# Performance work log

Hardware: AMD Instinct MI355X
Metric: run time of the kernel (lower is better)

The kernel has to match this reference:

```python
import jax, jax.numpy as jnp
import numpy as np

B, T, E, C, H = 8, 96, 96, 256, 8
D = C // H
HID = int(C * 4.0)
EPS = 1e-5


def _ln(x, g, b):
    m = x.mean(-1, keepdims=True)
    v = ((x - m) ** 2).mean(-1, keepdims=True)
    return (x - m) * jax.lax.rsqrt(v + EPS) * g + b


def setup_inputs() -> dict:
    key = jax.random.key(0)
    ks = jax.random.split(key, 20)
    s = 0.02
    inp = {
        "x": jax.random.normal(ks[0], (B, T, E, C), jnp.float32),
        "adj_mask": jax.random.uniform(ks[1], (E, E), jnp.float32) * 2.0 - 1.0,  # direction cosines in [-1,1]
        "n1_g": jnp.ones((C,)), "n1_b": jnp.zeros((C,)),
        "s_wq": jax.random.normal(ks[2], (C, C)) * s,
        "s_wk": jax.random.normal(ks[3], (C, C)) * s,
        "s_wv": jax.random.normal(ks[4], (C, C)) * s,
        "s_wp": jax.random.normal(ks[5], (C, C)) * s,
        "s_bp": jnp.zeros((C,)),
        "s_ng": jnp.ones((C,)), "s_nb": jnp.zeros((C,)),
        "s_gamma": jax.random.normal(ks[6], (1,)) * 0.1,
        "n2_g": jnp.ones((C,)), "n2_b": jnp.zeros((C,)),
        "t_wq": jax.random.normal(ks[7], (C, C)) * s,
        "t_wk": jax.random.normal(ks[8], (C, C)) * s,
        "t_wv": jax.random.normal(ks[9], (C, C)) * s,
        "t_wp": jax.random.normal(ks[10], (C, C)) * s,
        "t_bp": jnp.zeros((C,)),
        "t_gamma": jax.random.normal(ks[11], (1,)) * 0.1,
        "n3_g": jnp.ones((C,)), "n3_b": jnp.zeros((C,)),
        "m_w1": jax.random.normal(ks[12], (C, HID)) * s,
        "m_b1": jnp.zeros((HID,)),
        "m_w2": jax.random.normal(ks[13], (HID, C)) * s,
        "m_b2": jnp.zeros((C,)),
    }
    return inp


def _interp_linear_T(x, t_new):
    # x: [B, T, E, C]; torch F.interpolate(mode='linear', align_corners=False) over T
    t = x.shape[1]
    scale = t / t_new
    src = (jnp.arange(t_new, dtype=jnp.float32) + 0.5) * scale - 0.5
    src = jnp.clip(src, 0.0, t - 1)
    i0 = jnp.floor(src).astype(jnp.int32)
    i1 = jnp.minimum(i0 + 1, t - 1)
    w = (src - i0.astype(jnp.float32))[None, :, None, None]
    return x[:, i0] * (1.0 - w) + x[:, i1] * w


def reference(x, adj_mask, n1_g, n1_b, s_wq, s_wk, s_wv, s_wp, s_bp, s_ng, s_nb, s_gamma,
              n2_g, n2_b, t_wq, t_wk, t_wv, t_wp, t_bp, t_gamma,
              n3_g, n3_b, m_w1, m_b1, m_w2, m_b2):
    b, t, e, c = x.shape
    h, d = H, C // H

    # ---- spatial geometric-cosine attention (per frame) ----
    xs = _ln(x, n1_g, n1_b)                                    # identity inside spatial_attn
    q = (xs @ s_wq).reshape(b, t, e, h, d)
    k = (xs @ s_wk).reshape(b, t, e, h, d)
    v = (xs @ s_wv).reshape(b, t, e, h, d)
    attn = jnp.einsum('btqhd,btkhd->bthqk', q, k)
    attn = (attn * adj_mask + 1.0) * 0.5                        # masked-cosine, no softmax
    o = jnp.einsum('bthqk,btkhd->btqhd', attn, v).reshape(b, t, e, c)
    o = _ln(o @ s_wp + s_bp, s_ng, s_nb)
    x = x + (xs + s_gamma * o)

    # ---- temporal softmax attention (per edge) ----
    xt = _ln(x, n2_g, n2_b)
    q = (xt @ t_wq).reshape(b, t, e, h, d)
    k = (xt @ t_wk).reshape(b, t, e, h, d)
    v = (xt @ t_wv).reshape(b, t, e, h, d)
    attn = jnp.einsum('bqehd,bkehd->behqk', q, k) * (d ** -0.5)
    attn = jax.nn.softmax(attn, axis=-1)
    o = jnp.einsum('behqk,bkehd->bqehd', attn, v).reshape(b, t, e, c)
    o = o @ t_wp + t_bp
    x = x + t_gamma * o

    # ---- MLP ----
    xm = _ln(x, n3_g, n3_b)
    x = x + (jax.nn.gelu(xm @ m_w1 + m_b1, approximate=False) @ m_w2 + m_b2)

    # ---- temporal downsampling (interpolate) ----
    t_new = t // 2 + t % 2
    if t > 1:
        x = _interp_linear_T(x, t_new)
    return x
```

## Files before the change

### kernel.cpp

```cpp
#include <hip/hip_runtime.h>
#include <cmath>

constexpr int BB = 8, TT = 96, EE = 96, CC = 256, HHD = 8, DDm = 32;
constexpr int NTOK = BB * TT * EE;
constexpr int TOUT = TT / 2;

typedef unsigned short u16;
typedef short bf16x8 __attribute__((ext_vector_type(8)));
typedef float f32x4 __attribute__((ext_vector_type(4)));

__device__ __forceinline__ float bf2f(u16 u) {
  union { unsigned int i; float f; } v; v.i = ((unsigned int)u) << 16; return v.f;
}
__device__ __forceinline__ u16 f2bf(float f) {
  union { unsigned int i; float f; } v; v.f = f;
  return (u16)((v.i + 0x7FFFu + ((v.i >> 16) & 1u)) >> 16);
}
__device__ __forceinline__ float wsum(float v) {
#pragma unroll
  for (int off = 32; off; off >>= 1) v += __shfl_xor(v, off);
  return v;
}
__device__ __forceinline__ float gelu_f(float x) {
  return 0.5f * x * (1.0f + erff(x * 0.70710678118654752f));
}
__device__ __forceinline__ int remap_row(int row, int mode) {
  if (mode == 0) return row;
  int b = row / (TT * EE);
  int rem = row - b * (TT * EE);
  if (mode == 1) { int t = rem / EE, e = rem - t * EE; return (b * EE + e) * TT + t; }
  int e = rem / TT, t = rem - e * TT;
  return (b * TT + t) * EE + e;
}

struct WPtr8 { const float* p[8]; };
__global__ void k_transpose8(WPtr8 src, u16* __restrict__ dst) {
  const float* in = src.p[blockIdx.y];
  u16* out = dst + (size_t)blockIdx.y * 65536;
  int idx = blockIdx.x * 256 + threadIdx.x;
  int k = idx >> 8, c = idx & 255;
  out[c * 256 + k] = f2bf(in[idx]);
}

__global__ void k_transpose(const float* __restrict__ in, u16* __restrict__ out, int K, int Nc, int n) {
  int idx = blockIdx.x * 256 + threadIdx.x;
  if (idx < n) {
    int k = idx / Nc, c = idx - k * Nc;
    out[c * K + k] = f2bf(in[idx]);
  }
}

__global__ void k_cvt(const float* __restrict__ in, u16* __restrict__ out, int n) {
  int idx = blockIdx.x * 256 + threadIdx.x;
  if (idx < n) out[idx] = f2bf(in[idx]);
}

__global__ __launch_bounds__(256) void k_ln_in(const float* __restrict__ x,
                                               u16* __restrict__ A, const float* __restrict__ g,
                                               const float* __restrict__ b) {
  int wv = threadIdx.x >> 6, lane = threadIdx.x & 63;
  long tok = (long)blockIdx.x * 4 + wv;
  int c = lane * 4;
  long off = tok * CC + c;
  float4 v = *(const float4*)(x + off);
  float s = v.x + v.y + v.z + v.w;
  float sq = v.x * v.x + v.y * v.y + v.z * v.z + v.w * v.w;
  s = wsum(s); sq = wsum(sq);
  float m = s * (1.0f / CC);
  float rs = rsqrtf(sq * (1.0f / CC) - m * m + 1e-5f);
  float4 gv = *(const float4*)(g + c);
  float4 bv = *(const float4*)(b + c);
  ushort4 o;
  o.x = f2bf((v.x - m) * rs * gv.x + bv.x);
  o.y = f2bf((v.y - m) * rs * gv.y + bv.y);
  o.z = f2bf((v.z - m) * rs * gv.z + bv.z);
  o.w = f2bf((v.w - m) * rs * gv.w + bv.w);
  *(ushort4*)(A + off) = o;
}

__global__ __launch_bounds__(256) void k_ln_f32(const float* __restrict__ X, u16* __restrict__ A,
                                                const float* __restrict__ g, const float* __restrict__ b) {
  int wv = threadIdx.x >> 6, lane = threadIdx.x & 63;
  long tok = (long)blockIdx.x * 4 + wv;
  int c = lane * 4;
  long off = tok * CC + c;
  float4 v = *(const float4*)(X + off);
  float s = v.x + v.y + v.z + v.w;
  float sq = v.x * v.x + v.y * v.y + v.z * v.z + v.w * v.w;
  s = wsum(s); sq = wsum(sq);
  float m = s * (1.0f / CC);
  float rs = rsqrtf(sq * (1.0f / CC) - m * m + 1e-5f);
  float4 gv = *(const float4*)(g + c);
  float4 bv = *(const float4*)(b + c);
  ushort4 o;
  o.x = f2bf((v.x - m) * rs * gv.x + bv.x);
  o.y = f2bf((v.y - m) * rs * gv.y + bv.y);
  o.z = f2bf((v.z - m) * rs * gv.z + bv.z);
  o.w = f2bf((v.w - m) * rs * gv.w + bv.w);
  *(ushort4*)(A + off) = o;
}

__global__ __launch_bounds__(256) void k_sp_combine(const float* __restrict__ xin, float* __restrict__ X,
                                                    u16* __restrict__ A, const u16* __restrict__ P,
                                                    const float* __restrict__ n1g, const float* __restrict__ n1b,
                                                    const float* __restrict__ sg,
                                                    const float* __restrict__ s_ng, const float* __restrict__ s_nb,
                                                    const float* __restrict__ n2g, const float* __restrict__ n2b) {
  int wv = threadIdx.x >> 6, lane = threadIdx.x & 63;
  long tok = (long)blockIdx.x * 4 + wv;
  int c = lane * 4;
  long off = tok * CC + c;
  float4 xv = *(const float4*)(xin + off);
  float s1 = xv.x + xv.y + xv.z + xv.w;
  float q1 = xv.x * xv.x + xv.y * xv.y + xv.z * xv.z + xv.w * xv.w;
  s1 = wsum(s1); q1 = wsum(q1);
  float m1 = s1 * (1.0f / CC);
  float r1 = rsqrtf(q1 * (1.0f / CC) - m1 * m1 + 1e-5f);
  float4 g1 = *(const float4*)(n1g + c);
  float4 b1 = *(const float4*)(n1b + c);
  float xs0 = (xv.x - m1) * r1 * g1.x + b1.x;
  float xs1 = (xv.y - m1) * r1 * g1.y + b1.y;
  float xs2 = (xv.z - m1) * r1 * g1.z + b1.z;
  float xs3 = (xv.w - m1) * r1 * g1.w + b1.w;
  ushort4 up = *(const ushort4*)(P + off);
  float4 p = make_float4(bf2f(up.x), bf2f(up.y), bf2f(up.z), bf2f(up.w));
  float s = p.x + p.y + p.z + p.w;
  float sq = p.x * p.x + p.y * p.y + p.z * p.z + p.w * p.w;
  s = wsum(s); sq = wsum(sq);
  float m = s * (1.0f / CC);
  float rs = rsqrtf(sq * (1.0f / CC) - m * m + 1e-5f);
  float4 ug = *(const float4*)(s_ng + c);
  float4 ub = *(const float4*)(s_nb + c);
  float o0 = (p.x - m) * rs * ug.x + ub.x;
  float o1 = (p.y - m) * rs * ug.y + ub.y;
  float o2 = (p.z - m) * rs * ug.z + ub.z;
  float o3 = (p.w - m) * rs * ug.w + ub.w;
  float gsg = sg[0];
  float x0 = xv.x + xs0 + gsg * o0;
  float x1 = xv.y + xs1 + gsg * o1;
  float x2 = xv.z + xs2 + gsg * o2;
  float x3 = xv.w + xs3 + gsg * o3;
  *(float4*)(X + off) = make_float4(x0, x1, x2, x3);
  float s2 = x0 + x1 + x2 + x3;
  float sq2 = x0 * x0 + x1 * x1 + x2 * x2 + x3 * x3;
  s2 = wsum(s2); sq2 = wsum(sq2);
  float m2 = s2 * (1.0f / CC);
  float rs2 = rsqrtf(sq2 * (1.0f / CC) - m2 * m2 + 1e-5f);
  float4 g2 = *(const float4*)(n2g + c);
  float4 b2 = *(const float4*)(n2b + c);
  ushort4 o;
  o.x = f2bf((x0 - m2) * rs2 * g2.x + b2.x);
  o.y = f2bf((x1 - m2) * rs2 * g2.y + b2.y);
  o.z = f2bf((x2 - m2) * rs2 * g2.z + b2.z);
  o.w = f2bf((x3 - m2) * rs2 * g2.w + b2.w);
  *(ushort4*)(A + off) = o;
}

__global__ __launch_bounds__(256) void k_gemm128(const u16* __restrict__ act, const u16* __restrict__ Wt,
                                                 const float* __restrict__ bias, const float* __restrict__ gptr,
                                                 u16* __restrict__ outB, float* __restrict__ Xacc,
                                                 int Kd, int Nc, int lda, int ldb, int epi, int remap) {
  __shared__ __align__(16) u16 smem[3 * 8192];
  int gx = gridDim.x;
  int nwg = gx * gridDim.y;
  int lid = blockIdx.y * gx + blockIdx.x;
  if ((nwg & 7) == 0) lid = (lid & 7) * (nwg >> 3) + (lid >> 3);
  int m0 = (lid / gx) * 128, n0 = (lid % gx) * 128;
  int tid = threadIdx.x;
  int wv = tid >> 6, lane = tid & 63, lm = lane & 15, quad = lane >> 4;
  int wr = wv >> 1, wc = wv & 1;
  f32x4 acc[4][4];
#pragma unroll
  for (int i = 0; i < 4; i++)
#pragma unroll
    for (int j = 0; j < 4; j++) acc[i][j] = (f32x4){0.f, 0.f, 0.f, 0.f};

  int srow = tid >> 2;
  int sseg = (tid & 3) ^ ((srow >> 1) & 3);
  const u16* pa = act + (long)(m0 + srow) * lda + sseg * 8;
  const u16* pb = Wt + (long)(n0 + srow) * ldb + sseg * 8;

  auto STAGE = [&](int buf, int kk) {
    u16* sb = smem + buf * 8192;
#pragma unroll
    for (int j = 0; j < 2; j++) {
      __builtin_amdgcn_global_load_lds(pa + (long)j * 64 * lda + kk, sb + (j * 256 + wv * 64) * 8, 16, 0, 0);
      __builtin_amdgcn_global_load_lds(pb + (long)j * 64 * ldb + kk, sb + 4096 + (j * 256 + wv * 64) * 8, 16, 0, 0);
    }
  };

  int nsteps = Kd >> 5;
  STAGE(0, 0);
  STAGE(1, 32);
  asm volatile("s_waitcnt vmcnt(4)" ::: "memory");
  __builtin_amdgcn_sched_barrier(0);
  __builtin_amdgcn_s_barrier();

  int xsw = (lm >> 1) & 3;
  int cur = 0;
  for (int t = 0; t < nsteps; ++t) {
    if (t + 2 < nsteps) {
      int nb = cur + 2; if (nb >= 3) nb -= 3;
      STAGE(nb, (t + 2) << 5);
    }
    const u16* As = smem + cur * 8192;
    const u16* Bs = As + 4096;
    bf16x8 af[4], bfv[4];
#pragma unroll
    for (int q = 0; q < 4; q++) {
      af[q] = *(const bf16x8*)&As[(wr * 64 + q * 16 + lm) * 32 + (quad ^ xsw) * 8];
      bfv[q] = *(const bf16x8*)&Bs[(wc * 64 + q * 16 + lm) * 32 + (quad ^ xsw) * 8];
    }
    __builtin_amdgcn_s_setprio(1);
#pragma unroll
    for (int ti = 0; ti < 4; ti++)
#pragma unroll
      for (int tj = 0; tj < 4; tj++)
        acc[ti][tj] = __builtin_amdgcn_mfma_f32_16x16x32_bf16(af[ti], bfv[tj], acc[ti][tj], 0, 0, 0);
    __builtin_amdgcn_s_setprio(0);
    asm volatile("s_waitcnt lgkmcnt(0)" ::: "memory");
    __builtin_amdgcn_sched_barrier(0);
    if (t + 2 < nsteps) asm volatile("s_waitcnt vmcnt(4)" ::: "memory");
    else                asm volatile("s_waitcnt vmcnt(0)" ::: "memory");
    __builtin_amdgcn_sched_barrier(0);
    __builtin_amdgcn_s_barrier();
    cur += 1; if (cur >= 3) cur -= 3;
  }

  if (epi == 3) {
    float gm = gptr ? gptr[0] : 1.0f;
    float* fs = (float*)smem;
#pragma unroll
    for (int half = 0; half < 2; half++) {
      if (half) __syncthreads();
      if (wr == half) {
#pragma unroll
        for (int tj = 0; tj < 4; tj++) {
          int col = wc * 64 + tj * 16 + lm;
          float bv = bias ? bias[n0 + col] : 0.0f;
#pragma unroll
          for (int ti = 0; ti < 4; ti++)
#pragma unroll
            for (int r = 0; r < 4; r++)
              fs[(ti * 16 + quad * 4 + r) * 132 + col] = gm * (acc[ti][tj][r] + bv);
        }
      }
      __syncthreads();
#pragma unroll
      for (int p = 0; p < 8; p++) {
        int idx = p * 256 + tid;
        int row = idx >> 5, c4 = idx & 31;
        int grow = remap_row(m0 + half * 64 + row, remap);
        float* gp = Xacc + (long)grow * Nc + n0 + c4 * 4;
        float4 xv = *(float4*)gp;
        float4 sv = *(const float4*)&fs[row * 132 + c4 * 4];
        xv.x += sv.x; xv.y += sv.y; xv.z += sv.z; xv.w += sv.w;
        *(float4*)gp = xv;
      }
    }
  } else {
#pragma unroll
    for (int tj = 0; tj < 4; tj++) {
      int col = wc * 64 + tj * 16 + lm;
      float bv = (epi >= 1 && bias) ? bias[n0 + col] : 0.0f;
#pragma unroll
      for (int ti = 0; ti < 4; ti++)
#pragma unroll
        for (int r = 0; r < 4; r++) {
          float vv = acc[ti][tj][r] + bv;
          if (epi == 2) vv = gelu_f(vv);
          smem[(wr * 64 + ti * 16 + quad * 4 + r) * 136 + col] = f2bf(vv);
        }
    }
    __syncthreads();
#pragma unroll
    for (int p = 0; p < 8; p++) {
      int idx = p * 256 + tid;
      int row = idx >> 4, c8 = idx & 15;
      int grow = remap_row(m0 + row, remap);
      *(uint4*)(outB + (long)grow * Nc + n0 + c8 * 8) = *(const uint4*)&smem[row * 136 + c8 * 8];
    }
  }
}

__global__ __launch_bounds__(384) void k_sp_attn(const u16* __restrict__ QKV, const u16* __restrict__ adj,
                                                 u16* __restrict__ O) {
  __shared__ __align__(16) u16 Qs[96 * 32];
  __shared__ __align__(16) u16 Ks[96 * 32];
  __shared__ __align__(16) u16 Vt[32 * 104];
  __shared__ __align__(16) u16 Ss[96 * 104];
  int blk = blockIdx.x;
  blk = (blk & 7) * ((int)gridDim.x >> 3) + (blk >> 3);
  int t = blk % TT, b = blk / TT;
  long fQ = ((long)(b * TT + t) * EE) * 768;
  long fO = ((long)(b * TT + t) * EE) * CC;
  int tid = threadIdx.x;
  int row = tid >> 2, seg = tid & 3;
  int wv = tid >> 6, lane = tid & 63, lm = lane & 15, quad = lane >> 4;
  long gq0 = fQ + (long)row * 768 + seg * 8;
  uint4 rq = *(const uint4*)(QKV + gq0);
  uint4 rk = *(const uint4*)(QKV + gq0 + 256);
  uint4 rv = *(const uint4*)(QKV + gq0 + 512);
  int cb = seg * 24;
  for (int h = 0; h < 8; ++h) {
    *(uint4*)&Qs[row * 32 + seg * 8] = rq;
    *(uint4*)&Ks[row * 32 + seg * 8] = rk;
    { union { uint4 u; u16 s[8]; } vv; vv.u = rv;
#pragma unroll
      for (int i = 0; i < 8; i++) Vt[(seg * 8 + i) * 104 + row] = vv.s[i]; }
#pragma unroll
    for (int i = 0; i < 3; i++)
      *(uint4*)&Ss[row * 104 + cb + i * 8] = *(const uint4*)(adj + row * 96 + cb + i * 8);
    __syncthreads();
    if (h < 7) {
      long g = gq0 + (h + 1) * 32;
      rq = *(const uint4*)(QKV + g);
      rk = *(const uint4*)(QKV + g + 256);
      rv = *(const uint4*)(QKV + g + 512);
      __builtin_amdgcn_sched_barrier(0);
    }
    bf16x8 aq = *(const bf16x8*)&Qs[(wv * 16 + lm) * 32 + quad * 8];
    f32x4 sc[6];
#pragma unroll
    for (int j = 0; j < 6; j++) {
      bf16x8 bk = *(const bf16x8*)&Ks[(j * 16 + lm) * 32 + quad * 8];
      f32x4 z = (f32x4){0.f, 0.f, 0.f, 0.f};
      sc[j] = __builtin_amdgcn_mfma_f32_16x16x32_bf16(aq, bk, z, 0, 0, 0);
    }
    u16 sv[6][4];
#pragma unroll
    for (int j = 0; j < 6; j++) {
      int col = j * 16 + lm;
#pragma unroll
      for (int r = 0; r < 4; r++) {
        int rrow = wv * 16 + quad * 4 + r;
        float a = bf2f(Ss[rrow * 104 + col]);
        sv[j][r] = f2bf((sc[j][r] * a + 1.0f) * 0.5f);
      }
    }
    __syncthreads();
#pragma unroll
    for (int j = 0; j < 6; j++) {
      int col = j * 16 + lm;
#pragma unroll
      for (int r = 0; r < 4; r++) Ss[(wv * 16 + quad * 4 + r) * 104 + col] = sv[j][r];
    }
    __syncthreads();
    f32x4 oc[2];
    oc[0] = (f32x4){0.f, 0.f, 0.f, 0.f};
    oc[1] = (f32x4){0.f, 0.f, 0.f, 0.f};
#pragma unroll
    for (int ks = 0; ks < 3; ks++) {
      bf16x8 as = *(const bf16x8*)&Ss[(wv * 16 + lm) * 104 + ks * 32 + quad * 8];
#pragma unroll
      for (int n = 0; n < 2; n++) {
        bf16x8 bv = *(const bf16x8*)&Vt[(n * 16 + lm) * 104 + ks * 32 + quad * 8];
        oc[n] = __builtin_amdgcn_mfma_f32_16x16x32_bf16(as, bv, oc[n], 0, 0, 0);
      }
    }
#pragma unroll
    for (int n = 0; n < 2; n++)
#pragma unroll
      for (int r = 0; r < 4; r++) {
        int rrow = wv * 16 + quad * 4 + r;
        O[fO + (long)rrow * CC + h * DDm + n * 16 + lm] = f2bf(oc[n][r]);
      }
    __syncthreads();
  }
}

__global__ __launch_bounds__(384) void k_tp_attn(const u16* __restrict__ QKV, u16* __restrict__ O) {
  __shared__ __align__(16) u16 Qs[96 * 32];
  __shared__ __align__(16) u16 Ks[96 * 32];
  __shared__ __align__(16) u16 Vt[32 * 104];
  __shared__ __align__(16) u16 Ss[96 * 104];
  int blk = blockIdx.x;
  blk = (blk & 7) * ((int)gridDim.x >> 3) + (blk >> 3);
  int e = blk % EE, b = blk / EE;
  long fQ = ((long)(b * EE + e) * TT) * 768;
  long fO = ((long)(b * EE + e) * TT) * CC;
  int tid = threadIdx.x;
  int row = tid >> 2, seg = tid & 3;
  int wv = tid >> 6, lane = tid & 63, lm = lane & 15, quad = lane >> 4;
  long gq0 = fQ + (long)row * 768 + seg * 8;
  uint4 rq = *(const uint4*)(QKV + gq0);
  uint4 rk = *(const uint4*)(QKV + gq0 + 256);
  uint4 rv = *(const uint4*)(QKV + gq0 + 512);
  const float scale = 0.17677669529663687f;
  for (int h = 0; h < 8; ++h) {
    *(uint4*)&Qs[row * 32 + seg * 8] = rq;
    *(uint4*)&Ks[row * 32 + seg * 8] = rk;
    { union { uint4 u; u16 s[8]; } vv; vv.u = rv;
#pragma unroll
      for (int i = 0; i < 8; i++) Vt[(seg * 8 + i) * 104 + row] = vv.s[i]; }
    __syncthreads();
    if (h < 7) {
      long g = gq0 + (h + 1) * 32;
      rq = *(const uint4*)(QKV + g);
      rk = *(const uint4*)(QKV + g + 256);
      rv = *(const uint4*)(QKV + g + 512);
      __builtin_amdgcn_sched_barrier(0);
    }
    bf16x8 aq = *(const bf16x8*)&Qs[(wv * 16 + lm) * 32 + quad * 8];
    f32x4 sc[6];
#pragma unroll
    for (int j = 0; j < 6; j++) {
      bf16x8 bk = *(const bf16x8*)&Ks[(j * 16 + lm) * 32 + quad * 8];
      f32x4 z = (f32x4){0.f, 0.f, 0.f, 0.f};
      sc[j] = __builtin_amdgcn_mfma_f32_16x16x32_bf16(aq, bk, z, 0, 0, 0);
    }
#pragma unroll
    for (int r = 0; r < 4; r++) {
      float mx = -1e30f;
#pragma unroll
      for (int j = 0; j < 6; j++) { sc[j][r] *= scale; mx = fmaxf(mx, sc[j][r]); }
#pragma unroll
      for (int mask = 1; mask < 16; mask <<= 1) mx = fmaxf(mx, __shfl_xor(mx, mask));
      float sum = 0.f;
#pragma unroll
      for (int j = 0; j < 6; j++) { float p = __expf(sc[j][r] - mx); sc[j][r] = p; sum += p; }
#pragma unroll
      for (int mask = 1; mask < 16; mask <<= 1) sum += __shfl_xor(sum, mask);
      float inv = 1.0f / sum;
#pragma unroll
      for (int j = 0; j < 6; j++) sc[j][r] *= inv;
    }
#pragma unroll
    for (int j = 0; j < 6; j++) {
      int col = j * 16 + lm;
#pragma unroll
      for (int r = 0; r < 4; r++) Ss[(wv * 16 + quad * 4 + r) * 104 + col] = f2bf(sc[j][r]);
    }
    __syncthreads();
    f32x4 oc[2];
    oc[0] = (f32x4){0.f, 0.f, 0.f, 0.f};
    oc[1] = (f32x4){0.f, 0.f, 0.f, 0.f};
#pragma unroll
    for (int ks = 0; ks < 3; ks++) {
      bf16x8 as = *(const bf16x8*)&Ss[(wv * 16 + lm) * 104 + ks * 32 + quad * 8];
#pragma unroll
      for (int n = 0; n < 2; n++) {
        bf16x8 bv = *(const bf16x8*)&Vt[(n * 16 + lm) * 104 + ks * 32 + quad * 8];
        oc[n] = __builtin_amdgcn_mfma_f32_16x16x32_bf16(as, bv, oc[n], 0, 0, 0);
      }
    }
#pragma unroll
    for (int n = 0; n < 2; n++)
#pragma unroll
      for (int r = 0; r < 4; r++) {
        int rrow = wv * 16 + quad * 4 + r;
        O[fO + (long)rrow * CC + h * DDm + n * 16 + lm] = f2bf(oc[n][r]);
      }
    __syncthreads();
  }
}

__global__ __launch_bounds__(256) void k_down(const float* __restrict__ X, float* __restrict__ out) {
  long i4 = ((long)blockIdx.x * 256 + threadIdx.x) * 4;
  long tmp = i4;
  int c = (int)(tmp & 255); tmp >>= 8;
  int e = (int)(tmp % EE); tmp /= EE;
  int i = (int)(tmp % TOUT);
  int b = (int)(tmp / TOUT);
  long src0 = (((long)b * TT + 2 * i) * EE + e) * CC + c;
  float4 a = *(const float4*)(X + src0);
  float4 bb = *(const float4*)(X + src0 + (long)EE * CC);
  float4 o = make_float4(0.5f * (a.x + bb.x), 0.5f * (a.y + bb.y),
                         0.5f * (a.z + bb.z), 0.5f * (a.w + bb.w));
  *(float4*)(out + i4) = o;
}

extern "C" void kernel_launch(void* const* d_in, const int* in_sizes, int n_in,
                              void* d_out, int out_size, void* d_ws, size_t ws_size,
                              hipStream_t stream) {
  (void)in_sizes; (void)n_in; (void)out_size; (void)ws_size;
  const float* x   = (const float*)d_in[0];
  const float* adj = (const float*)d_in[1];
  const float* n1g = (const float*)d_in[2];
  const float* n1b = (const float*)d_in[3];
  const float* swq = (const float*)d_in[4];
  const float* swk = (const float*)d_in[5];
  const float* swv = (const float*)d_in[6];
  const float* swp = (const float*)d_in[7];
  const float* sbp = (const float*)d_in[8];
  const float* sng = (const float*)d_in[9];
  const float* snb = (const float*)d_in[10];
  const float* sg  = (const float*)d_in[11];
  const float* n2g = (const float*)d_in[12];
  const float* n2b = (const float*)d_in[13];
  const float* twq = (const float*)d_in[14];
  const float* twk = (const float*)d_in[15];
  const float* twv = (const float*)d_in[16];
  const float* twp = (const float*)d_in[17];
  const float* tbp = (const float*)d_in[18];
  const float* tg  = (const float*)d_in[19];
  const float* n3g = (const float*)d_in[20];
  const float* n3b = (const float*)d_in[21];
  const float* mw1 = (const float*)d_in[22];
  const float* mb1 = (const float*)d_in[23];
  const float* mw2 = (const float*)d_in[24];
  const float* mb2 = (const float*)d_in[25];
  float* out = (float*)d_out;

  size_t nc = (size_t)NTOK * CC;
  float* X  = (float*)d_ws;
  u16* A    = (u16*)(X + nc);
  u16* QKV  = A + nc;
  u16* Pb   = QKV;
  u16* Hh   = QKV;
  u16* wts  = QKV + 3 * nc;
  u16* swq_t = wts;
  u16* swp_t = wts + 3 * 65536;
  u16* twq_t = wts + 4 * 65536;
  u16* twp_t = wts + 7 * 65536;
  u16* w1_t  = wts + 8 * 65536;
  u16* w2_t  = w1_t + 262144;
  u16* adj_b = w2_t + 262144;

  WPtr8 w8; w8.p[0] = swq; w8.p[1] = swk; w8.p[2] = swv; w8.p[3] = swp;
  w8.p[4] = twq; w8.p[5] = twk; w8.p[6] = twv; w8.p[7] = twp;
  k_transpose8<<<dim3(256, 8), 256, 0, stream>>>(w8, wts);
  k_transpose<<<(256 * 1024 + 255) / 256, 256, 0, stream>>>(mw1, w1_t, 256, 1024, 256 * 1024);
  k_transpose<<<(1024 * 256 + 255) / 256, 256, 0, stream>>>(mw2, w2_t, 1024, 256, 1024 * 256);
  k_cvt<<<(EE * EE + 255) / 256, 256, 0, stream>>>(adj, adj_b, EE * EE);

  auto gemm = [&](const u16* act, const u16* Wt, const float* bias, const float* gamma,
                  u16* outB, float* Xacc, int Kd, int Nc, int lda, int ldb, int epi, int remap, int M) {
    dim3 g(Nc / 128, M / 128);
    k_gemm128<<<g, 256, 0, stream>>>(act, Wt, bias, gamma, outB, Xacc, Kd, Nc, lda, ldb, epi, remap);
  };

  int lnBlocks = NTOK / 4;

  k_ln_in<<<lnBlocks, 256, 0, stream>>>(x, A, n1g, n1b);
  gemm(A, swq_t, nullptr, nullptr, QKV, nullptr, 256, 768, 256, 256, 0, 0, NTOK);
  k_sp_attn<<<BB * TT, 384, 0, stream>>>(QKV, adj_b, A);
  gemm(A, swp_t, sbp, nullptr, Pb, nullptr, 256, 256, 256, 256, 1, 0, NTOK);
  k_sp_combine<<<lnBlocks, 256, 0, stream>>>(x, X, A, Pb, n1g, n1b, sg, sng, snb, n2g, n2b);

  gemm(A, twq_t, nullptr, nullptr, QKV, nullptr, 256, 768, 256, 256, 0, 1, NTOK);
  k_tp_attn<<<BB * EE, 384, 0, stream>>>(QKV, A);
  gemm(A, twp_t, tbp, tg, nullptr, X, 256, 256, 256, 256, 3, 2, NTOK);

  k_ln_f32<<<lnBlocks, 256, 0, stream>>>(X, A, n3g, n3b);
  for (int hf = 0; hf < 2; hf++) {
    long r0 = (long)hf * (NTOK / 2);
    gemm(A + r0 * CC, w1_t, mb1, nullptr, Hh, nullptr, 256, 1024, 256, 256, 2, 0, NTOK / 2);
    gemm(Hh, w2_t, mb2, nullptr, nullptr, X + r0 * CC, 1024, 256, 1024, 1024, 3, 0, NTOK / 2);
  }

  long outElems = (long)BB * TOUT * EE * CC;
  k_down<<<(int)(outElems / 4 / 256), 256, 0, stream>>>(X, out);
}
```

Measured before the change: 699.7 us.

## Replace 128x128 GEMM with 256x256-tile, 512-thread double-buffered GEMM

Swaps the 128x128 bf16 MFMA GEMM (3-stage, K-step 32) for a 256x256 tile kernel with 8 waves, K-step 64 and double buffering, using a new XOR swizzle on 64-wide LDS rows. B fragments are loaded once per K-step and reused across four sub-passes over A, with barriers between sub-passes. The epilogues are reworked to write the larger tile in halves or quarters through LDS. The goal is more reuse per byte loaded and fewer workgroups. The cost is 128 KB of LDS per block, lower occupancy, and fewer blocks for the N=256 GEMMs, which could hurt latency hiding.

```diff
diff --git a/kernel.cpp b/kernel.cpp
--- a/kernel.cpp
+++ b/kernel.cpp
@@ -156,129 +156,146 @@
   *(ushort4*)(A + off) = o;
 }
 
-__global__ __launch_bounds__(256) void k_gemm128(const u16* __restrict__ act, const u16* __restrict__ Wt,
-                                                 const float* __restrict__ bias, const float* __restrict__ gptr,
-                                                 u16* __restrict__ outB, float* __restrict__ Xacc,
-                                                 int Kd, int Nc, int lda, int ldb, int epi, int remap) {
-  __shared__ __align__(16) u16 smem[3 * 8192];
+__global__ __launch_bounds__(512, 2) void k_gemm256(const u16* __restrict__ act, const u16* __restrict__ Wt,
+                                                    const float* __restrict__ bias, const float* __restrict__ gptr,
+                                                    u16* __restrict__ outB, float* __restrict__ Xacc,
+                                                    int Kd, int Nc, int lda, int ldb, int epi, int remap) {
+  __shared__ __align__(16) u16 smem[2 * 32768];
   int gx = gridDim.x;
   int nwg = gx * gridDim.y;
   int lid = blockIdx.y * gx + blockIdx.x;
   if ((nwg & 7) == 0) lid = (lid & 7) * (nwg >> 3) + (lid >> 3);
-  int m0 = (lid / gx) * 128, n0 = (lid % gx) * 128;
+  int m0 = (lid / gx) * 256, n0 = (lid % gx) * 256;
   int tid = threadIdx.x;
-  int wv = tid >> 6, lane = tid & 63, lm = lane & 15, quad = lane >> 4;
-  int wr = wv >> 1, wc = wv & 1;
-  f32x4 acc[4][4];
-#pragma unroll
-  for (int i = 0; i < 4; i++)
+  int wid = tid >> 6, lane = tid & 63, lm = lane & 15, quad = lane >> 4;
+  int wm = wid >> 2, wn = wid & 3;
+  f32x4 acc[8][4];
+#pragma unroll
+  for (int i = 0; i < 8; i++)
 #pragma unroll
     for (int j = 0; j < 4; j++) acc[i][j] = (f32x4){0.f, 0.f, 0.f, 0.f};
 
-  int srow = tid >> 2;
-  int sseg = (tid & 3) ^ ((srow >> 1) & 3);
-  const u16* pa = act + (long)(m0 + srow) * lda + sseg * 8;
-  const u16* pb = Wt + (long)(n0 + srow) * ldb + sseg * 8;
+  int srow = wid * 8 + (lane >> 3);
+  int swsl = (lane & 7) ^ (lane >> 3);
+  const u16* pa = act + (long)(m0 + srow) * lda + swsl * 8;
+  const u16* pb = Wt + (long)(n0 + srow) * ldb + swsl * 8;
 
   auto STAGE = [&](int buf, int kk) {
-    u16* sb = smem + buf * 8192;
-#pragma unroll
-    for (int j = 0; j < 2; j++) {
-      __builtin_amdgcn_global_load_lds(pa + (long)j * 64 * lda + kk, sb + (j * 256 + wv * 64) * 8, 16, 0, 0);
-      __builtin_amdgcn_global_load_lds(pb + (long)j * 64 * ldb + kk, sb + 4096 + (j * 256 + wv * 64) * 8, 16, 0, 0);
+    u16* sb = smem + buf * 32768;
+#pragma unroll
+    for (int j = 0; j < 4; j++) {
+      __builtin_amdgcn_global_load_lds(pa + (long)(j * 64) * lda + kk, sb + (j * 64 + wid * 8) * 64, 16, 0, 0);
+      __builtin_amdgcn_global_load_lds(pb + (long)(j * 64) * ldb + kk, sb + 16384 + (j * 64 + wid * 8) * 64, 16, 0, 0);
     }
   };
 
-  int nsteps = Kd >> 5;
+  int NT = Kd >> 6;
   STAGE(0, 0);
-  STAGE(1, 32);
-  asm volatile("s_waitcnt vmcnt(4)" ::: "memory");
+  asm volatile("s_waitcnt vmcnt(0)" ::: "memory");
   __builtin_amdgcn_sched_barrier(0);
   __builtin_amdgcn_s_barrier();
 
-  int xsw = (lm >> 1) & 3;
+  int swk = lm & 7;
   int cur = 0;
-  for (int t = 0; t < nsteps; ++t) {
-    if (t + 2 < nsteps) {
-      int nb = cur + 2; if (nb >= 3) nb -= 3;
-      STAGE(nb, (t + 2) << 5);
-    }
-    const u16* As = smem + cur * 8192;
-    const u16* Bs = As + 4096;
-    bf16x8 af[4], bfv[4];
-#pragma unroll
-    for (int q = 0; q < 4; q++) {
-      af[q] = *(const bf16x8*)&As[(wr * 64 + q * 16 + lm) * 32 + (quad ^ xsw) * 8];
-      bfv[q] = *(const bf16x8*)&Bs[(wc * 64 + q * 16 + lm) * 32 + (quad ^ xsw) * 8];
-    }
-    __builtin_amdgcn_s_setprio(1);
-#pragma unroll
-    for (int ti = 0; ti < 4; ti++)
-#pragma unroll
-      for (int tj = 0; tj < 4; tj++)
-        acc[ti][tj] = __builtin_amdgcn_mfma_f32_16x16x32_bf16(af[ti], bfv[tj], acc[ti][tj], 0, 0, 0);
-    __builtin_amdgcn_s_setprio(0);
-    asm volatile("s_waitcnt lgkmcnt(0)" ::: "memory");
-    __builtin_amdgcn_sched_barrier(0);
-    if (t + 2 < nsteps) asm volatile("s_waitcnt vmcnt(4)" ::: "memory");
-    else                asm volatile("s_waitcnt vmcnt(0)" ::: "memory");
+  for (int t = 0; t < NT; ++t) {
+    if (t + 1 < NT) STAGE(cur ^ 1, (t + 1) << 6);
+    const u16* As = smem + cur * 32768;
+    const u16* Bs = As + 16384;
+    bf16x8 bfr[4][2];
+#pragma unroll
+    for (int nf = 0; nf < 4; nf++)
+#pragma unroll
+      for (int ks = 0; ks < 2; ks++)
+        bfr[nf][ks] = *(const bf16x8*)&Bs[(wn * 64 + nf * 16 + lm) * 64 + (((ks * 4 + quad) ^ swk) * 8)];
+#pragma unroll
+    for (int p = 0; p < 4; p++) {
+      bf16x8 af[2][2];
+#pragma unroll
+      for (int mi = 0; mi < 2; mi++)
+#pragma unroll
+        for (int ks = 0; ks < 2; ks++)
+          af[mi][ks] = *(const bf16x8*)&As[(wm * 128 + (p * 2 + mi) * 16 + lm) * 64 + (((ks * 4 + quad) ^ swk) * 8)];
+      __builtin_amdgcn_s_barrier();
+      asm volatile("s_waitcnt lgkmcnt(0)" ::: "memory");
+      __builtin_amdgcn_sched_barrier(0);
+      __builtin_amdgcn_s_setprio(1);
+#pragma unroll
+      for (int ks = 0; ks < 2; ks++)
+#pragma unroll
+        for (int mi = 0; mi < 2; mi++)
+#pragma unroll
+          for (int nf = 0; nf < 4; nf++)
+            acc[p * 2 + mi][nf] = __builtin_amdgcn_mfma_f32_16x16x32_bf16(af[mi][ks], bfr[nf][ks],
+                                                                          acc[p * 2 + mi][nf], 0, 0, 0);
+      __builtin_amdgcn_s_setprio(0);
+      if (p < 3) __builtin_amdgcn_s_barrier();
+    }
+    asm volatile("s_waitcnt vmcnt(0)" ::: "memory");
     __builtin_amdgcn_sched_barrier(0);
     __builtin_amdgcn_s_barrier();
-    cur += 1; if (cur >= 3) cur -= 3;
+    cur ^= 1;
   }
 
   if (epi == 3) {
     float gm = gptr ? gptr[0] : 1.0f;
     float* fs = (float*)smem;
 #pragma unroll
-    for (int half = 0; half < 2; half++) {
-      if (half) __syncthreads();
-      if (wr == half) {
-#pragma unroll
-        for (int tj = 0; tj < 4; tj++) {
-          int col = wc * 64 + tj * 16 + lm;
+    for (int qp = 0; qp < 4; qp++) {
+      if (qp) __syncthreads();
+      if (wm == (qp >> 1)) {
+        int mfb = (qp & 1) * 4;
+#pragma unroll
+        for (int nf = 0; nf < 4; nf++) {
+          int col = wn * 64 + nf * 16 + lm;
           float bv = bias ? bias[n0 + col] : 0.0f;
 #pragma unroll
-          for (int ti = 0; ti < 4; ti++)
+          for (int mi = 0; mi < 4; mi++)
 #pragma unroll
             for (int r = 0; r < 4; r++)
-              fs[(ti * 16 + quad * 4 + r) * 132 + col] = gm * (acc[ti][tj][r] + bv);
+              fs[(mi * 16 + quad * 4 + r) * 264 + col] = gm * (acc[mfb + mi][nf][r] + bv);
         }
       }
       __syncthreads();
 #pragma unroll
-      for (int p = 0; p < 8; p++) {
-        int idx = p * 256 + tid;
-        int row = idx >> 5, c4 = idx & 31;
-        int grow = remap_row(m0 + half * 64 + row, remap);
+      for (int p2 = 0; p2 < 8; p2++) {
+        int idx = p2 * 512 + tid;
+        int lrow = idx >> 6, c4 = idx & 63;
+        int grow = remap_row(m0 + qp * 64 + lrow, remap);
         float* gp = Xacc + (long)grow * Nc + n0 + c4 * 4;
         float4 xv = *(float4*)gp;
-        float4 sv = *(const float4*)&fs[row * 132 + c4 * 4];
+        float4 sv = *(const float4*)&fs[lrow * 264 + c4 * 4];
         xv.x += sv.x; xv.y += sv.y; xv.z += sv.z; xv.w += sv.w;
         *(float4*)gp = xv;
       }
     }
   } else {
-#pragma unroll
-    for (int tj = 0; tj < 4; tj++) {
-      int col = wc * 64 + tj * 16 + lm;
-      float bv = (epi >= 1 && bias) ? bias[n0 + col] : 0.0f;
-#pragma unroll
-      for (int ti = 0; ti < 4; ti++)
-#pragma unroll
-        for (int r = 0; r < 4; r++) {
-          float vv = acc[ti][tj][r] + bv;
-          if (epi == 2) vv = gelu_f(vv);
-          smem[(wr * 64 + ti * 16 + quad * 4 + r) * 136 + col] = f2bf(vv);
+    u16* fs = smem;
+#pragma unroll
+    for (int h = 0; h < 2; h++) {
+      if (h) __syncthreads();
+      if (wm == h) {
+#pragma unroll
+        for (int nf = 0; nf < 4; nf++) {
+          int col = wn * 64 + nf * 16 + lm;
+          float bv = (epi >= 1 && bias) ? bias[n0 + col] : 0.0f;
+#pragma unroll
+          for (int mf = 0; mf < 8; mf++)
+#pragma unroll
+            for (int r = 0; r < 4; r++) {
+              float vv = acc[mf][nf][r] + bv;
+              if (epi == 2) vv = gelu_f(vv);
+              fs[(mf * 16 + quad * 4 + r) * 264 + col] = f2bf(vv);
+            }
         }
-    }
-    __syncthreads();
-#pragma unroll
-    for (int p = 0; p < 8; p++) {
-      int idx = p * 256 + tid;
-      int row = idx >> 4, c8 = idx & 15;
-      int grow = remap_row(m0 + row, remap);
-      *(uint4*)(outB + (long)grow * Nc + n0 + c8 * 8) = *(const uint4*)&smem[row * 136 + c8 * 8];
+      }
+      __syncthreads();
+#pragma unroll
+      for (int p2 = 0; p2 < 8; p2++) {
+        int idx = p2 * 512 + tid;
+        int lrow = idx >> 5, c8 = idx & 31;
+        int grow = remap_row(m0 + h * 128 + lrow, remap);
+        *(uint4*)(outB + (long)grow * Nc + n0 + c8 * 8) = *(const uint4*)&fs[lrow * 264 + c8 * 8];
+      }
     }
   }
 }
@@ -526,8 +543,8 @@
 
   auto gemm = [&](const u16* act, const u16* Wt, const float* bias, const float* gamma,
                   u16* outB, float* Xacc, int Kd, int Nc, int lda, int ldb, int epi, int remap, int M) {
-    dim3 g(Nc / 128, M / 128);
-    k_gemm128<<<g, 256, 0, stream>>>(act, Wt, bias, gamma, outB, Xacc, Kd, Nc, lda, ldb, epi, remap);
+    dim3 g(Nc / 256, M / 256);
+    k_gemm256<<<g, 512, 0, stream>>>(act, Wt, bias, gamma, outB, Xacc, Kd, Nc, lda, ldb, epi, remap);
   };
 
   int lnBlocks = NTOK / 4;
```

Result: slower. 1.107 ms (+58.2%).

## Fuse spatial output projection GEMM with layernorm-combine epilogue

Applied to the files above, without the earlier changes.

Replaces the spatial projection GEMM and the separate combine kernel with one kernel. Each block computes a full 128x256 row tile of the projection, stages it in shared memory, then runs the residual add and the three layernorms in-block. This removes the write and re-read of the bf16 projection buffer and one launch. Each block writes A in place, which is safe because it reads only its own 128 rows before writing them. The cost is a larger shared-memory footprint and fewer blocks per CU.

```diff
diff --git a/kernel.cpp b/kernel.cpp
--- a/kernel.cpp
+++ b/kernel.cpp
@@ -100,62 +100,6 @@
   *(ushort4*)(A + off) = o;
 }
 
-__global__ __launch_bounds__(256) void k_sp_combine(const float* __restrict__ xin, float* __restrict__ X,
-                                                    u16* __restrict__ A, const u16* __restrict__ P,
-                                                    const float* __restrict__ n1g, const float* __restrict__ n1b,
-                                                    const float* __restrict__ sg,
-                                                    const float* __restrict__ s_ng, const float* __restrict__ s_nb,
-                                                    const float* __restrict__ n2g, const float* __restrict__ n2b) {
-  int wv = threadIdx.x >> 6, lane = threadIdx.x & 63;
-  long tok = (long)blockIdx.x * 4 + wv;
-  int c = lane * 4;
-  long off = tok * CC + c;
-  float4 xv = *(const float4*)(xin + off);
-  float s1 = xv.x + xv.y + xv.z + xv.w;
-  float q1 = xv.x * xv.x + xv.y * xv.y + xv.z * xv.z + xv.w * xv.w;
-  s1 = wsum(s1); q1 = wsum(q1);
-  float m1 = s1 * (1.0f / CC);
-  float r1 = rsqrtf(q1 * (1.0f / CC) - m1 * m1 + 1e-5f);
-  float4 g1 = *(const float4*)(n1g + c);
-  float4 b1 = *(const float4*)(n1b + c);
-  float xs0 = (xv.x - m1) * r1 * g1.x + b1.x;
-  float xs1 = (xv.y - m1) * r1 * g1.y + b1.y;
-  float xs2 = (xv.z - m1) * r1 * g1.z + b1.z;
-  float xs3 = (xv.w - m1) * r1 * g1.w + b1.w;
-  ushort4 up = *(const ushort4*)(P + off);
-  float4 p = make_float4(bf2f(up.x), bf2f(up.y), bf2f(up.z), bf2f(up.w));
-  float s = p.x + p.y + p.z + p.w;
-  float sq = p.x * p.x + p.y * p.y + p.z * p.z + p.w * p.w;
-  s = wsum(s); sq = wsum(sq);
-  float m = s * (1.0f / CC);
-  float rs = rsqrtf(sq * (1.0f / CC) - m * m + 1e-5f);
-  float4 ug = *(const float4*)(s_ng + c);
-  float4 ub = *(const float4*)(s_nb + c);
-  float o0 = (p.x - m) * rs * ug.x + ub.x;
-  float o1 = (p.y - m) * rs * ug.y + ub.y;
-  float o2 = (p.z - m) * rs * ug.z + ub.z;
-  float o3 = (p.w - m) * rs * ug.w + ub.w;
-  float gsg = sg[0];
-  float x0 = xv.x + xs0 + gsg * o0;
-  float x1 = xv.y + xs1 + gsg * o1;
-  float x2 = xv.z + xs2 + gsg * o2;
-  float x3 = xv.w + xs3 + gsg * o3;
-  *(float4*)(X + off) = make_float4(x0, x1, x2, x3);
-  float s2 = x0 + x1 + x2 + x3;
-  float sq2 = x0 * x0 + x1 * x1 + x2 * x2 + x3 * x3;
-  s2 = wsum(s2); sq2 = wsum(sq2);
-  float m2 = s2 * (1.0f / CC);
-  float rs2 = rsqrtf(sq2 * (1.0f / CC) - m2 * m2 + 1e-5f);
-  float4 g2 = *(const float4*)(n2g + c);
-  float4 b2 = *(const float4*)(n2b + c);
-  ushort4 o;
-  o.x = f2bf((x0 - m2) * rs2 * g2.x + b2.x);
-  o.y = f2bf((x1 - m2) * rs2 * g2.y + b2.y);
-  o.z = f2bf((x2 - m2) * rs2 * g2.z + b2.z);
-  o.w = f2bf((x3 - m2) * rs2 * g2.w + b2.w);
-  *(ushort4*)(A + off) = o;
-}
-
 __global__ __launch_bounds__(256) void k_gemm128(const u16* __restrict__ act, const u16* __restrict__ Wt,
                                                  const float* __restrict__ bias, const float* __restrict__ gptr,
                                                  u16* __restrict__ outB, float* __restrict__ Xacc,
@@ -280,6 +224,144 @@
       int grow = remap_row(m0 + row, remap);
       *(uint4*)(outB + (long)grow * Nc + n0 + c8 * 8) = *(const uint4*)&smem[row * 136 + c8 * 8];
     }
+  }
+}
+
+__global__ __launch_bounds__(512, 2) void k_projcmb(const u16* __restrict__ act, const u16* __restrict__ Wt,
+                                                    const float* __restrict__ bias,
+                                                    const float* __restrict__ xin, float* __restrict__ X,
+                                                    u16* __restrict__ Aout,
+                                                    const float* __restrict__ n1g, const float* __restrict__ n1b,
+                                                    const float* __restrict__ sg,
+                                                    const float* __restrict__ s_ng, const float* __restrict__ s_nb,
+                                                    const float* __restrict__ n2g, const float* __restrict__ n2b) {
+  __shared__ __align__(16) u16 smem[3 * 12288];
+  int nwg = gridDim.x;
+  int lid = blockIdx.x;
+  lid = (lid & 7) * (nwg >> 3) + (lid >> 3);
+  int m0 = lid * 128;
+  int tid = threadIdx.x;
+  int wid = tid >> 6, lane = tid & 63, lm = lane & 15, quad = lane >> 4;
+  int wm = wid >> 2, wn = wid & 3;
+  f32x4 acc[4][4];
+#pragma unroll
+  for (int i = 0; i < 4; i++)
+#pragma unroll
+    for (int j = 0; j < 4; j++) acc[i][j] = (f32x4){0.f, 0.f, 0.f, 0.f};
+
+  int srow = tid >> 2;
+  int sseg = (tid & 3) ^ ((tid >> 3) & 3);
+  const u16* pa = act + (long)(m0 + srow) * CC + sseg * 8;
+  const u16* pb = Wt + (long)srow * CC + sseg * 8;
+
+  auto STAGE = [&](int buf, int kk) {
+    u16* sa = smem + buf * 12288;
+    u16* sb = sa + 4096;
+    __builtin_amdgcn_global_load_lds(pa + kk, sa + (wid * 64) * 8, 16, 0, 0);
+#pragma unroll
+    for (int j = 0; j < 2; j++)
+      __builtin_amdgcn_global_load_lds(pb + (long)(j * 128) * CC + kk, sb + (j * 512 + wid * 64) * 8, 16, 0, 0);
+  };
+
+  STAGE(0, 0);
+  STAGE(1, 32);
+  asm volatile("s_waitcnt vmcnt(3)" ::: "memory");
+  __builtin_amdgcn_sched_barrier(0);
+  __builtin_amdgcn_s_barrier();
+
+  int xsw = (lm >> 1) & 3;
+  int cur = 0;
+#pragma unroll
+  for (int t = 0; t < 8; ++t) {
+    if (t + 2 < 8) {
+      int nb = cur + 2; if (nb >= 3) nb -= 3;
+      STAGE(nb, (t + 2) << 5);
+    }
+    const u16* As = smem + cur * 12288;
+    const u16* Bs = As + 4096;
+    bf16x8 af[4], bfv[4];
+#pragma unroll
+    for (int q = 0; q < 4; q++) {
+      af[q] = *(const bf16x8*)&As[(wm * 64 + q * 16 + lm) * 32 + (quad ^ xsw) * 8];
+      bfv[q] = *(const bf16x8*)&Bs[(wn * 64 + q * 16 + lm) * 32 + (quad ^ xsw) * 8];
+    }
+    __builtin_amdgcn_s_setprio(1);
+#pragma unroll
+    for (int ti = 0; ti < 4; ti++)
+#pragma unroll
+      for (int tj = 0; tj < 4; tj++)
+        acc[ti][tj] = __builtin_amdgcn_mfma_f32_16x16x32_bf16(af[ti], bfv[tj], acc[ti][tj], 0, 0, 0);
+    __builtin_amdgcn_s_setprio(0);
+    asm volatile("s_waitcnt lgkmcnt(0)" ::: "memory");
+    __builtin_amdgcn_sched_barrier(0);
+    if (t + 2 < 8) asm volatile("s_waitcnt vmcnt(3)" ::: "memory");
+    else           asm volatile("s_waitcnt vmcnt(0)" ::: "memory");
+    __builtin_amdgcn_sched_barrier(0);
+    __builtin_amdgcn_s_barrier();
+    cur += 1; if (cur >= 3) cur -= 3;
+  }
+
+  u16* Cs = smem;
+#pragma unroll
+  for (int tj = 0; tj < 4; tj++) {
+    int col = wn * 64 + tj * 16 + lm;
+    float bv = bias[col];
+#pragma unroll
+    for (int ti = 0; ti < 4; ti++)
+#pragma unroll
+      for (int r = 0; r < 4; r++)
+        Cs[(wm * 64 + ti * 16 + quad * 4 + r) * 264 + col] = f2bf(acc[ti][tj][r] + bv);
+  }
+  __syncthreads();
+
+  int c = lane * 4;
+  float4 g1 = *(const float4*)(n1g + c);
+  float4 b1 = *(const float4*)(n1b + c);
+  float4 ug = *(const float4*)(s_ng + c);
+  float4 ub = *(const float4*)(s_nb + c);
+  float4 g2 = *(const float4*)(n2g + c);
+  float4 b2 = *(const float4*)(n2b + c);
+  float gsg = sg[0];
+  for (int rr = 0; rr < 16; ++rr) {
+    int row = wid * 16 + rr;
+    long off = (long)(m0 + row) * CC + c;
+    float4 xv = *(const float4*)(xin + off);
+    float s1 = xv.x + xv.y + xv.z + xv.w;
+    float q1 = xv.x * xv.x + xv.y * xv.y + xv.z * xv.z + xv.w * xv.w;
+    s1 = wsum(s1); q1 = wsum(q1);
+    float m1 = s1 * (1.0f / CC);
+    float r1 = rsqrtf(q1 * (1.0f / CC) - m1 * m1 + 1e-5f);
+    float xs0 = (xv.x - m1) * r1 * g1.x + b1.x;
+    float xs1 = (xv.y - m1) * r1 * g1.y + b1.y;
+    float xs2 = (xv.z - m1) * r1 * g1.z + b1.z;
+    float xs3 = (xv.w - m1) * r1 * g1.w + b1.w;
+    ushort4 up = *(const ushort4*)&Cs[row * 264 + c];
+    float4 p = make_float4(bf2f(up.x), bf2f(up.y), bf2f(up.z), bf2f(up.w));
+    float s = p.x + p.y + p.z + p.w;
+    float sq = p.x * p.x + p.y * p.y + p.z * p.z + p.w * p.w;
+    s = wsum(s); sq = wsum(sq);
+    float m = s * (1.0f / CC);
+    float rs = rsqrtf(sq * (1.0f / CC) - m * m + 1e-5f);
+    float o0 = (p.x - m) * rs * ug.x + ub.x;
+    float o1 = (p.y - m) * rs * ug.y + ub.y;
+    float o2 = (p.z - m) * rs * ug.z + ub.z;
+    float o3 = (p.w - m) * rs * ug.w + ub.w;
+    float x0 = xv.x + xs0 + gsg * o0;
+    float x1 = xv.y + xs1 + gsg * o1;
+    float x2 = xv.z + xs2 + gsg * o2;
+    float x3 = xv.w + xs3 + gsg * o3;
+    *(float4*)(X + off) = make_float4(x0, x1, x2, x3);
+    float s2 = x0 + x1 + x2 + x3;
+    float sq2 = x0 * x0 + x1 * x1 + x2 * x2 + x3 * x3;
+    s2 = wsum(s2); sq2 = wsum(sq2);
+    float m2 = s2 * (1.0f / CC);
+    float rs2 = rsqrtf(sq2 * (1.0f / CC) - m2 * m2 + 1e-5f);
+    ushort4 o;
+    o.x = f2bf((x0 - m2) * rs2 * g2.x + b2.x);
+    o.y = f2bf((x1 - m2) * rs2 * g2.y + b2.y);
+    o.z = f2bf((x2 - m2) * rs2 * g2.z + b2.z);
+    o.w = f2bf((x3 - m2) * rs2 * g2.w + b2.w);
+    *(ushort4*)(Aout + off) = o;
   }
 }
 
@@ -506,7 +588,6 @@
   float* X  = (float*)d_ws;
   u16* A    = (u16*)(X + nc);
   u16* QKV  = A + nc;
-  u16* Pb   = QKV;
   u16* Hh   = QKV;
   u16* wts  = QKV + 3 * nc;
   u16* swq_t = wts;
@@ -535,8 +616,8 @@
   k_ln_in<<<lnBlocks, 256, 0, stream>>>(x, A, n1g, n1b);
   gemm(A, swq_t, nullptr, nullptr, QKV, nullptr, 256, 768, 256, 256, 0, 0, NTOK);
   k_sp_attn<<<BB * TT, 384, 0, stream>>>(QKV, adj_b, A);
-  gemm(A, swp_t, sbp, nullptr, Pb, nullptr, 256, 256, 256, 256, 1, 0, NTOK);
-  k_sp_combine<<<lnBlocks, 256, 0, stream>>>(x, X, A, Pb, n1g, n1b, sg, sng, snb, n2g, n2b);
+  k_projcmb<<<NTOK / 128, 512, 0, stream>>>(A, swp_t, sbp, x, X, A,
+                                            n1g, n1b, sg, sng, snb, n2g, n2b);
 
   gemm(A, twq_t, nullptr, nullptr, QKV, nullptr, 256, 768, 256, 256, 0, 1, NTOK);
   k_tp_attn<<<BB * EE, 384, 0, stream>>>(QKV, A);
```

New measurement: 682.5 us. 2.4% less time.
